# Kernel tuning notes

Measured on AMD Instinct MI355X. Metric: run time of the kernel, lower is better.

The kernel has to match this reference:

```python
import jax, jax.numpy as jnp
import numpy as np

H = 8  # num heads
LORA_SCALE = 1.0


def _lora(x, down, up):
    # down: [rank, in], up: [out, rank]; sigma_mask is None -> ones -> no-op
    return (x @ down.T) @ up.T


def setup_inputs() -> dict:
    key = jax.random.key(0)
    ks = jax.random.split(key, 16)
    B, S, C = 16, 1024, 1280
    Senc, Cenc = 77, 1024
    rank = 4
    s = lambda n: 1.0 / np.sqrt(n)
    inp = {
        "hidden_states": jax.random.normal(ks[0], (B, S, C), jnp.float32),
        "encoder_hidden_states": jax.random.normal(ks[1], (B, Senc, Cenc), jnp.float32),
        "Wq": jax.random.normal(ks[2], (C, C), jnp.float32) * s(C),
        "Wk": jax.random.normal(ks[3], (C, Cenc), jnp.float32) * s(Cenc),
        "Wv": jax.random.normal(ks[4], (C, Cenc), jnp.float32) * s(Cenc),
        "Wo": jax.random.normal(ks[5], (C, C), jnp.float32) * s(C),
        "bo": jnp.zeros((C,), jnp.float32),
        "q_down": jax.random.normal(ks[6], (rank, C), jnp.float32) / rank,
        "q_up": jax.random.normal(ks[7], (C, rank), jnp.float32) * 0.02,
        "k_down": jax.random.normal(ks[8], (rank, Cenc), jnp.float32) / rank,
        "k_up": jax.random.normal(ks[9], (C, rank), jnp.float32) * 0.02,
        "v_down": jax.random.normal(ks[10], (rank, Cenc), jnp.float32) / rank,
        "v_up": jax.random.normal(ks[11], (C, rank), jnp.float32) * 0.02,
        "o_down": jax.random.normal(ks[12], (rank, C), jnp.float32) / rank,
        "o_up": jax.random.normal(ks[13], (C, rank), jnp.float32) * 0.02,
    }
    return inp


def reference(hidden_states, encoder_hidden_states, Wq, Wk, Wv, Wo, bo,
              q_down, q_up, k_down, k_up, v_down, v_up, o_down, o_up):
    B, S, C = hidden_states.shape
    Senc = encoder_hidden_states.shape[1]
    D = C // H
    attn_scale = 1.0 / jnp.sqrt(jnp.asarray(D, hidden_states.dtype))

    q = hidden_states @ Wq.T + LORA_SCALE * _lora(hidden_states, q_down, q_up)
    k = encoder_hidden_states @ Wk.T + LORA_SCALE * _lora(encoder_hidden_states, k_down, k_up)
    v = encoder_hidden_states @ Wv.T + LORA_SCALE * _lora(encoder_hidden_states, v_down, v_up)

    # head_to_batch_dim: [B, S, H*D] -> [B, H, S, D]
    q = q.reshape(B, S, H, D).transpose(0, 2, 1, 3)
    k = k.reshape(B, Senc, H, D).transpose(0, 2, 1, 3)
    v = v.reshape(B, Senc, H, D).transpose(0, 2, 1, 3)

    scores = jnp.einsum("bhqd,bhkd->bhqk", q, k) * attn_scale
    probs = jax.nn.softmax(scores, axis=-1)
    out = jnp.einsum("bhqk,bhkd->bhqd", probs, v)

    # batch_to_head_dim: [B, H, S, D] -> [B, S, H*D]
    out = out.transpose(0, 2, 1, 3).reshape(B, S, C)
    out = out @ Wo.T + bo + LORA_SCALE * _lora(out, o_down, o_up)
    return out
```

## Files before the change

### kernel.cpp

```cpp
#include <hip/hip_runtime.h>

#define NH    8
#define BB    16
#define SQ    1024
#define CC    1280
#define SENC  77
#define CENC  1024
#define DH    160
#define RANK  4

typedef __attribute__((ext_vector_type(8))) short bf16x8;
typedef __attribute__((ext_vector_type(4))) float f32x4;

__device__ inline void split_bf16(float a, unsigned short& hi, unsigned short& lo) {
    unsigned u = __float_as_uint(a);
    hi = (unsigned short)(u >> 16);
    float fhi = __uint_as_float(u & 0xffff0000u);
    float r = a - fhi;
    lo = (unsigned short)(__float_as_uint(r) >> 16);
}

__global__ void fold_kernel(const float* __restrict__ W,
                            const float* __restrict__ up,
                            const float* __restrict__ down,
                            float* __restrict__ out, int N, int K) {
    int idx4 = blockIdx.x * blockDim.x + threadIdx.x;
    int total4 = (N * K) >> 2;
    if (idx4 >= total4) return;
    int i = idx4 << 2;
    int n = i / K;
    int kk = i - n * K;
    float4 acc = *(const float4*)(W + i);
#pragma unroll
    for (int r = 0; r < RANK; ++r) {
        float u = up[n * RANK + r];
        float4 dv = *(const float4*)(down + (size_t)r * K + kk);
        acc.x += u * dv.x; acc.y += u * dv.y;
        acc.z += u * dv.z; acc.w += u * dv.w;
    }
    *(float4*)(out + i) = acc;
}

__global__ void fold_split_kernel(const float* __restrict__ W,
                                  const float* __restrict__ up,
                                  const float* __restrict__ down,
                                  unsigned short* __restrict__ ohi,
                                  unsigned short* __restrict__ olo,
                                  int N, int K) {
    int idx4 = blockIdx.x * blockDim.x + threadIdx.x;
    int total4 = (N * K) >> 2;
    if (idx4 >= total4) return;
    int i = idx4 << 2;
    int n = i / K;
    int kk = i - n * K;
    float4 acc = *(const float4*)(W + i);
#pragma unroll
    for (int r = 0; r < RANK; ++r) {
        float u = up[n * RANK + r];
        float4 dv = *(const float4*)(down + (size_t)r * K + kk);
        acc.x += u * dv.x; acc.y += u * dv.y;
        acc.z += u * dv.z; acc.w += u * dv.w;
    }
    unsigned short h0, h1, h2, h3, l0, l1, l2, l3;
    split_bf16(acc.x, h0, l0); split_bf16(acc.y, h1, l1);
    split_bf16(acc.z, h2, l2); split_bf16(acc.w, h3, l3);
    int2 hv, lv;
    hv.x = (int)((unsigned)h0 | ((unsigned)h1 << 16));
    hv.y = (int)((unsigned)h2 | ((unsigned)h3 << 16));
    lv.x = (int)((unsigned)l0 | ((unsigned)l1 << 16));
    lv.y = (int)((unsigned)l2 | ((unsigned)l3 << 16));
    *(int2*)(ohi + i) = hv;
    *(int2*)(olo + i) = lv;
}

__global__ void split_kernel(const float* __restrict__ x,
                             unsigned short* __restrict__ ohi,
                             unsigned short* __restrict__ olo, int total4) {
    int idx4 = blockIdx.x * blockDim.x + threadIdx.x;
    if (idx4 >= total4) return;
    int i = idx4 << 2;
    float4 a = *(const float4*)(x + i);
    unsigned short h0, h1, h2, h3, l0, l1, l2, l3;
    split_bf16(a.x, h0, l0); split_bf16(a.y, h1, l1);
    split_bf16(a.z, h2, l2); split_bf16(a.w, h3, l3);
    int2 hv, lv;
    hv.x = (int)((unsigned)h0 | ((unsigned)h1 << 16));
    hv.y = (int)((unsigned)h2 | ((unsigned)h3 << 16));
    lv.x = (int)((unsigned)l0 | ((unsigned)l1 << 16));
    lv.y = (int)((unsigned)l2 | ((unsigned)l3 << 16));
    *(int2*)(ohi + i) = hv;
    *(int2*)(olo + i) = lv;
}

__global__ __launch_bounds__(256) void transpose_split_kernel(
    const float* __restrict__ in,
    unsigned short* __restrict__ ohi, unsigned short* __restrict__ olo) {
    __shared__ float t[32][33];
    int tx = threadIdx.x & 31, ty = threadIdx.x >> 5;
    int bx = blockIdx.x, by = blockIdx.y;
#pragma unroll
    for (int r = 0; r < 4; ++r)
        t[ty + 8 * r][tx] = in[(size_t)(by * 32 + ty + 8 * r) * 1280 + bx * 32 + tx];
    __syncthreads();
#pragma unroll
    for (int r = 0; r < 4; ++r) {
        float v = t[tx][ty + 8 * r];
        unsigned short h_, l_;
        split_bf16(v, h_, l_);
        size_t o = (size_t)(bx * 32 + ty + 8 * r) * 1280 + by * 32 + tx;
        ohi[o] = h_; olo[o] = l_;
    }
}

#define GBM 128
#define GBN 128
#define GBK 32

__device__ inline void async_load16(const void* gsrc, void* lds_dst) {
    __builtin_amdgcn_global_load_lds(
        (const __attribute__((address_space(1))) void*)gsrc,
        (__attribute__((address_space(3))) void*)lds_dst, 16, 0, 0);
}

__device__ inline int clampi(int x, int hi) { return x > hi ? hi : x; }

template <int MODE>
__global__ __launch_bounds__(256) void gemm2_kernel(
    const unsigned short* __restrict__ A_hi, const unsigned short* __restrict__ A_lo,
    int lda,
    const unsigned short* __restrict__ W_hi, const unsigned short* __restrict__ W_lo,
    int ldw,
    const float* __restrict__ bias, float* __restrict__ outF,
    unsigned short* __restrict__ oHi, unsigned short* __restrict__ oLo, int ldo,
    int M, int N, int K) {
    __shared__ __align__(16) unsigned short lds[4][GBM][GBK];
    const int tid  = threadIdx.x;
    const int wave = tid >> 6;
    const int lane = tid & 63;

    int m0, n0;
    if constexpr (MODE == 0) {
        n0 = blockIdx.x * GBN; m0 = blockIdx.y * GBM;
    } else if constexpr (MODE == 1) {
        n0 = blockIdx.x * GBN; m0 = 0;
        int z = blockIdx.z, b = z >> 3, hh = z & 7;
        size_t ao = (size_t)(b * SENC) * lda + hh * DH;
        A_hi += ao; A_lo += ao;
        W_hi += hh * DH; W_lo += hh * DH;
        size_t ob = (size_t)(b * 640 + hh * 80) * ldo;
        oHi += ob; oLo += ob;
    } else if constexpr (MODE == 2) {
        n0 = 0; m0 = blockIdx.y * GBM;
        int z = blockIdx.z, b = z >> 3, hh = z & 7;
        A_hi += hh * DH; A_lo += hh * DH;
        size_t wo = (size_t)(b * SENC) * ldw + CC + hh * DH;
        W_hi += wo; W_lo += wo;
        size_t ob = (size_t)b * CC * ldo + hh * 80;
        oHi += ob; oLo += ob;
    } else if constexpr (MODE == 3) {
        int bid = blockIdx.x;
        int w = (bid & 7) * 80 + (bid >> 3);
        int mt = w / 5, nt = w - mt * 5;
        m0 = mt * GBM; n0 = nt * GBN;
        int b = m0 >> 10;
        size_t wo = (size_t)b * 640 * ldw;
        W_hi += wo; W_lo += wo;
    } else {
        int bid = blockIdx.x;
        int w = (bid & 7) * 160 + (bid >> 3);
        int mt = w / 10, nt = w - mt * 10;
        m0 = mt * GBM; n0 = nt * GBN;
        int b = m0 >> 10;
        size_t wo = (size_t)b * CC * ldw;
        W_hi += wo; W_lo += wo;
    }

    const int wr = wave >> 1, wc = wave & 1;
    f32x4 zero = {0.f, 0.f, 0.f, 0.f};
    f32x4 acc[4][4];
#pragma unroll
    for (int i = 0; i < 4; ++i)
#pragma unroll
        for (int j = 0; j < 4; ++j) acc[i][j] = zero;

    const int c0 = wave * 2, c1 = wave * 2 + 1;
    const int rr = lane >> 2;
    const int kc = (lane & 3) * 8;
    const int ra0 = clampi(m0 + c0 * 16 + rr, M - 1);
    const int ra1 = clampi(m0 + c1 * 16 + rr, M - 1);
    const int rw0 = clampi(n0 + c0 * 16 + rr, N - 1);
    const int rw1 = clampi(n0 + c1 * 16 + rr, N - 1);
    const unsigned short* pAh0 = A_hi + (size_t)ra0 * lda + kc;
    const unsigned short* pAh1 = A_hi + (size_t)ra1 * lda + kc;
    const unsigned short* pAl0 = A_lo + (size_t)ra0 * lda + kc;
    const unsigned short* pAl1 = A_lo + (size_t)ra1 * lda + kc;
    const unsigned short* pWh0 = W_hi + (size_t)rw0 * ldw + kc;
    const unsigned short* pWh1 = W_hi + (size_t)rw1 * ldw + kc;
    const unsigned short* pWl0 = W_lo + (size_t)rw0 * ldw + kc;
    const unsigned short* pWl1 = W_lo + (size_t)rw1 * ldw + kc;

    for (int k0 = 0; k0 < K; k0 += GBK) {
        async_load16(pAh0 + k0, &lds[0][c0 * 16][0]);
        async_load16(pAh1 + k0, &lds[0][c1 * 16][0]);
        async_load16(pAl0 + k0, &lds[1][c0 * 16][0]);
        async_load16(pAl1 + k0, &lds[1][c1 * 16][0]);
        async_load16(pWh0 + k0, &lds[2][c0 * 16][0]);
        async_load16(pWh1 + k0, &lds[2][c1 * 16][0]);
        async_load16(pWl0 + k0, &lds[3][c0 * 16][0]);
        async_load16(pWl1 + k0, &lds[3][c1 * 16][0]);
        __syncthreads();

        bf16x8 ah[4], al[4], bh[4], bl[4];
        const int fr = lane & 15;
        const int kb = (lane >> 4) * 8;
#pragma unroll
        for (int i = 0; i < 4; ++i) {
            ah[i] = *(const bf16x8*)&lds[0][wr * 64 + i * 16 + fr][kb];
            al[i] = *(const bf16x8*)&lds[1][wr * 64 + i * 16 + fr][kb];
            bh[i] = *(const bf16x8*)&lds[2][wc * 64 + i * 16 + fr][kb];
            bl[i] = *(const bf16x8*)&lds[3][wc * 64 + i * 16 + fr][kb];
        }
#pragma unroll
        for (int i = 0; i < 4; ++i)
#pragma unroll
            for (int j = 0; j < 4; ++j) {
                acc[i][j] = __builtin_amdgcn_mfma_f32_16x16x32_bf16(ah[i], bh[j], acc[i][j], 0, 0, 0);
                acc[i][j] = __builtin_amdgcn_mfma_f32_16x16x32_bf16(ah[i], bl[j], acc[i][j], 0, 0, 0);
                acc[i][j] = __builtin_amdgcn_mfma_f32_16x16x32_bf16(al[i], bh[j], acc[i][j], 0, 0, 0);
            }
        __syncthreads();
    }

    const int fc = lane & 15;
    const int fr4 = (lane >> 4) * 4;
#pragma unroll
    for (int j = 0; j < 4; ++j) {
        int col = n0 + wc * 64 + j * 16 + fc;
        float bv = 0.f;
        if constexpr (MODE == 4) bv = bias[col];
#pragma unroll
        for (int i = 0; i < 4; ++i) {
            int row = m0 + wr * 64 + i * 16 + fr4;
#pragma unroll
            for (int r = 0; r < 4; ++r) {
                int rowr = row + r;
                float val = acc[i][j][r];
                if constexpr (MODE == 0) {
                    if (rowr < M) {
                        unsigned short vh, vl;
                        split_bf16(val, vh, vl);
                        oHi[(size_t)rowr * ldo + col] = vh;
                        oLo[(size_t)rowr * ldo + col] = vl;
                    }
                } else if constexpr (MODE == 1) {
                    if (rowr < 80) {
                        if (rowr >= SENC) val = 0.f;
                        unsigned short vh, vl;
                        split_bf16(val, vh, vl);
                        oHi[(size_t)rowr * ldo + col] = vh;
                        oLo[(size_t)rowr * ldo + col] = vl;
                    }
                } else if constexpr (MODE == 2) {
                    if (col < 80) {
                        if (col >= SENC) val = 0.f;
                        unsigned short vh, vl;
                        split_bf16(val, vh, vl);
                        oHi[(size_t)rowr * ldo + col] = vh;
                        oLo[(size_t)rowr * ldo + col] = vl;
                    }
                } else if constexpr (MODE == 3) {
                    outF[(size_t)rowr * ldo + col] = val;
                } else {
                    outF[(size_t)rowr * ldo + col] = val + bv;
                }
            }
        }
    }
}

__global__ __launch_bounds__(256) void softmax_kernel(
    const float* __restrict__ S,
    unsigned short* __restrict__ Phi, unsigned short* __restrict__ Plo) {
    const float scale = 0.07905694150420949f;
    int t = blockIdx.x * 256 + threadIdx.x;
    int li = t & 3;
    int g = t >> 2;
    int row = g >> 3, h = g & 7;
    const float* p = S + (size_t)row * 640 + h * 80;

    float v[20];
#pragma unroll
    for (int m = 0; m < 5; ++m) {
        float4 x = *(const float4*)(p + (li + 4 * m) * 4);
        v[m * 4 + 0] = x.x; v[m * 4 + 1] = x.y;
        v[m * 4 + 2] = x.z; v[m * 4 + 3] = x.w;
    }
    float mx = -1e30f;
#pragma unroll
    for (int m = 0; m < 5; ++m)
#pragma unroll
        for (int e = 0; e < 4; ++e) {
            int j = (li + 4 * m) * 4 + e;
            float x = v[m * 4 + e] * scale;
            v[m * 4 + e] = x;
            if (j < SENC) mx = fmaxf(mx, x);
        }
    mx = fmaxf(mx, __shfl_xor(mx, 1));
    mx = fmaxf(mx, __shfl_xor(mx, 2));
    float sum = 0.f;
#pragma unroll
    for (int m = 0; m < 5; ++m)
#pragma unroll
        for (int e = 0; e < 4; ++e) {
            int j = (li + 4 * m) * 4 + e;
            float ex = (j < SENC) ? __expf(v[m * 4 + e] - mx) : 0.f;
            v[m * 4 + e] = ex;
            sum += ex;
        }
    sum += __shfl_xor(sum, 1);
    sum += __shfl_xor(sum, 2);
    float inv = 1.f / sum;

    size_t ob = (size_t)row * 640 + h * 80;
#pragma unroll
    for (int m = 0; m < 5; ++m) {
        unsigned short hh[4], ll[4];
#pragma unroll
        for (int e = 0; e < 4; ++e) split_bf16(v[m * 4 + e] * inv, hh[e], ll[e]);
        ushort4 hv; hv.x = hh[0]; hv.y = hh[1]; hv.z = hh[2]; hv.w = hh[3];
        ushort4 lv; lv.x = ll[0]; lv.y = ll[1]; lv.z = ll[2]; lv.w = ll[3];
        *(ushort4*)(Phi + ob + (li + 4 * m) * 4) = hv;
        *(ushort4*)(Plo + ob + (li + 4 * m) * 4) = lv;
    }
}

extern "C" void kernel_launch(void* const* d_in, const int* in_sizes, int n_in,
                              void* d_out, int out_size, void* d_ws, size_t ws_size,
                              hipStream_t stream) {
    const float* hidden = (const float*)d_in[0];
    const float* enc    = (const float*)d_in[1];
    const float* Wq     = (const float*)d_in[2];
    const float* Wk     = (const float*)d_in[3];
    const float* Wv     = (const float*)d_in[4];
    const float* Wo     = (const float*)d_in[5];
    const float* bo     = (const float*)d_in[6];
    const float* q_down = (const float*)d_in[7];
    const float* q_up   = (const float*)d_in[8];
    const float* k_down = (const float*)d_in[9];
    const float* k_up   = (const float*)d_in[10];
    const float* v_down = (const float*)d_in[11];
    const float* v_up   = (const float*)d_in[12];
    const float* o_down = (const float*)d_in[13];
    const float* o_up   = (const float*)d_in[14];

    char* ws = (char*)d_ws;
    unsigned short* Wo_hi   = (unsigned short*)(ws);
    unsigned short* Wo_lo   = (unsigned short*)(ws + 3276800);
    unsigned short* kv_hi   = (unsigned short*)(ws + 6553600);
    unsigned short* kv_lo   = (unsigned short*)(ws + 12861440);
    unsigned short* Wkv_hi  = (unsigned short*)(ws + 19169280);
    unsigned short* Wkv_lo  = (unsigned short*)(ws + 24412160);
    unsigned short* Nbig_hi = (unsigned short*)(ws + 19169280);
    unsigned short* Nbig_lo = (unsigned short*)(ws + 45383680);
    unsigned short* P_hi    = (unsigned short*)(ws + 19169280);
    unsigned short* P_lo    = (unsigned short*)(ws + 40140800);
    unsigned short* MbT_hi  = (unsigned short*)(ws + 61112320);
    unsigned short* MbT_lo  = (unsigned short*)(ws + 87326720);
    float*          S_f32   = (float*)(ws + 71598080);
    unsigned short* WqT_hi  = (unsigned short*)(ws + 71598080);
    unsigned short* WqT_lo  = (unsigned short*)(ws + 74874880);
    float*          Wq_f32  = (float*)(ws + 78151680);
    unsigned short* enc_hi  = (unsigned short*)(ws + 84705280);
    unsigned short* enc_lo  = (unsigned short*)(ws + 87228416);
    unsigned short* hid_hi  = (unsigned short*)d_out;
    unsigned short* hid_lo  = hid_hi + (size_t)20971520;

    const int M1 = BB * SQ;
    const int M2 = BB * SENC;

    dim3 blk(256);
    fold_split_kernel<<<1600, blk, 0, stream>>>(Wo, o_up, o_down, Wo_hi, Wo_lo, CC, CC);
    fold_kernel<<<1600, blk, 0, stream>>>(Wq, q_up, q_down, Wq_f32, CC, CC);
    transpose_split_kernel<<<dim3(40, 40), blk, 0, stream>>>(Wq_f32, WqT_hi, WqT_lo);
    fold_split_kernel<<<1280, blk, 0, stream>>>(Wk, k_up, k_down, Wkv_hi, Wkv_lo, CC, CENC);
    fold_split_kernel<<<1280, blk, 0, stream>>>(Wv, v_up, v_down,
                                                Wkv_hi + 1310720, Wkv_lo + 1310720, CC, CENC);
    split_kernel<<<1232, blk, 0, stream>>>(enc, enc_hi, enc_lo, (M2 * CENC) / 4);
    split_kernel<<<20480, blk, 0, stream>>>(hidden, hid_hi, hid_lo, (M1 * CC) / 4);

    gemm2_kernel<0><<<dim3(20, 10), blk, 0, stream>>>(
        enc_hi, enc_lo, CENC, Wkv_hi, Wkv_lo, CENC,
        nullptr, nullptr, kv_hi, kv_lo, 2560, M2, 2560, CENC);

    gemm2_kernel<1><<<dim3(10, 1, 128), blk, 0, stream>>>(
        kv_hi, kv_lo, 2560, WqT_hi, WqT_lo, CC,
        nullptr, nullptr, Nbig_hi, Nbig_lo, CC, SENC, CC, DH);

    gemm2_kernel<3><<<640, blk, 0, stream>>>(
        hid_hi, hid_lo, CC, Nbig_hi, Nbig_lo, CC,
        nullptr, S_f32, nullptr, nullptr, 640, M1, 640, CC);

    softmax_kernel<<<2048, blk, 0, stream>>>(S_f32, P_hi, P_lo);

    gemm2_kernel<2><<<dim3(1, 10, 128), blk, 0, stream>>>(
        Wo_hi, Wo_lo, CC, kv_hi, kv_lo, 2560,
        nullptr, nullptr, MbT_hi, MbT_lo, 640, CC, SENC, DH);

    gemm2_kernel<4><<<1280, blk, 0, stream>>>(
        P_hi, P_lo, 640, MbT_hi, MbT_lo, 640,
        bo, (float*)d_out, nullptr, nullptr, CC, M1, CC, 640);
}
```

Baseline: 527.9 us.

## Fuse score GEMM with softmax and merge weight fold/transpose prep kernels

Replaces the separate score GEMM (which wrote fp32 scores) and the softmax kernel with one kernel. It uses 128x160 tiles so each wave owns a full 80-wide head segment and applies softmax in registers, removing the fp32 score round-trip through global memory. It also fuses the Wq LoRA fold into the transpose-split kernel and merges the K/V folds into one launch, saving launches and an intermediate buffer. The trade-off is larger per-thread accumulators (4x5 tiles) and more LDS, which may lower occupancy, plus scattered 2-byte stores for P.

```diff
diff --git a/kernel.cpp b/kernel.cpp
--- a/kernel.cpp
+++ b/kernel.cpp
@@ -18,27 +18,6 @@
     float fhi = __uint_as_float(u & 0xffff0000u);
     float r = a - fhi;
     lo = (unsigned short)(__float_as_uint(r) >> 16);
-}
-
-__global__ void fold_kernel(const float* __restrict__ W,
-                            const float* __restrict__ up,
-                            const float* __restrict__ down,
-                            float* __restrict__ out, int N, int K) {
-    int idx4 = blockIdx.x * blockDim.x + threadIdx.x;
-    int total4 = (N * K) >> 2;
-    if (idx4 >= total4) return;
-    int i = idx4 << 2;
-    int n = i / K;
-    int kk = i - n * K;
-    float4 acc = *(const float4*)(W + i);
-#pragma unroll
-    for (int r = 0; r < RANK; ++r) {
-        float u = up[n * RANK + r];
-        float4 dv = *(const float4*)(down + (size_t)r * K + kk);
-        acc.x += u * dv.x; acc.y += u * dv.y;
-        acc.z += u * dv.z; acc.w += u * dv.w;
-    }
-    *(float4*)(out + i) = acc;
 }
 
 __global__ void fold_split_kernel(const float* __restrict__ W,
@@ -71,6 +50,69 @@
     lv.y = (int)((unsigned)l2 | ((unsigned)l3 << 16));
     *(int2*)(ohi + i) = hv;
     *(int2*)(olo + i) = lv;
+}
+
+__global__ void fold_split_kv_kernel(const float* __restrict__ Wk,
+                                     const float* __restrict__ Wv,
+                                     const float* __restrict__ k_up,
+                                     const float* __restrict__ k_down,
+                                     const float* __restrict__ v_up,
+                                     const float* __restrict__ v_down,
+                                     unsigned short* __restrict__ ohi,
+                                     unsigned short* __restrict__ olo) {
+    int idx4 = blockIdx.x * blockDim.x + threadIdx.x;
+    int i = idx4 << 2;
+    int n = i >> 10;
+    int kk = i & 1023;
+    const float* W; const float* up; const float* down; int nn = n;
+    if (n < CC) { W = Wk; up = k_up; down = k_down; }
+    else        { W = Wv; up = v_up; down = v_down; nn = n - CC; }
+    float4 acc = *(const float4*)(W + (size_t)nn * CENC + kk);
+#pragma unroll
+    for (int r = 0; r < RANK; ++r) {
+        float u = up[nn * RANK + r];
+        float4 dv = *(const float4*)(down + (size_t)r * CENC + kk);
+        acc.x += u * dv.x; acc.y += u * dv.y;
+        acc.z += u * dv.z; acc.w += u * dv.w;
+    }
+    unsigned short h0, h1, h2, h3, l0, l1, l2, l3;
+    split_bf16(acc.x, h0, l0); split_bf16(acc.y, h1, l1);
+    split_bf16(acc.z, h2, l2); split_bf16(acc.w, h3, l3);
+    int2 hv, lv;
+    hv.x = (int)((unsigned)h0 | ((unsigned)h1 << 16));
+    hv.y = (int)((unsigned)h2 | ((unsigned)h3 << 16));
+    lv.x = (int)((unsigned)l0 | ((unsigned)l1 << 16));
+    lv.y = (int)((unsigned)l2 | ((unsigned)l3 << 16));
+    *(int2*)(ohi + i) = hv;
+    *(int2*)(olo + i) = lv;
+}
+
+__global__ __launch_bounds__(256) void foldT_split_kernel(
+    const float* __restrict__ W, const float* __restrict__ up,
+    const float* __restrict__ down,
+    unsigned short* __restrict__ ohi, unsigned short* __restrict__ olo) {
+    __shared__ float t[32][33];
+    int tx = threadIdx.x & 31, ty = threadIdx.x >> 5;
+    int bx = blockIdx.x, by = blockIdx.y;
+    int k = bx * 32 + tx;
+#pragma unroll
+    for (int r4 = 0; r4 < 4; ++r4) {
+        int n = by * 32 + ty + 8 * r4;
+        float v = W[(size_t)n * 1280 + k];
+#pragma unroll
+        for (int r = 0; r < RANK; ++r)
+            v += up[n * RANK + r] * down[r * 1280 + k];
+        t[ty + 8 * r4][tx] = v;
+    }
+    __syncthreads();
+#pragma unroll
+    for (int r4 = 0; r4 < 4; ++r4) {
+        float v = t[tx][ty + 8 * r4];
+        unsigned short h_, l_;
+        split_bf16(v, h_, l_);
+        size_t o = (size_t)(bx * 32 + ty + 8 * r4) * 1280 + by * 32 + tx;
+        ohi[o] = h_; olo[o] = l_;
+    }
 }
 
 __global__ void split_kernel(const float* __restrict__ x,
@@ -90,26 +132,6 @@
     lv.y = (int)((unsigned)l2 | ((unsigned)l3 << 16));
     *(int2*)(ohi + i) = hv;
     *(int2*)(olo + i) = lv;
-}
-
-__global__ __launch_bounds__(256) void transpose_split_kernel(
-    const float* __restrict__ in,
-    unsigned short* __restrict__ ohi, unsigned short* __restrict__ olo) {
-    __shared__ float t[32][33];
-    int tx = threadIdx.x & 31, ty = threadIdx.x >> 5;
-    int bx = blockIdx.x, by = blockIdx.y;
-#pragma unroll
-    for (int r = 0; r < 4; ++r)
-        t[ty + 8 * r][tx] = in[(size_t)(by * 32 + ty + 8 * r) * 1280 + bx * 32 + tx];
-    __syncthreads();
-#pragma unroll
-    for (int r = 0; r < 4; ++r) {
-        float v = t[tx][ty + 8 * r];
-        unsigned short h_, l_;
-        split_bf16(v, h_, l_);
-        size_t o = (size_t)(bx * 32 + ty + 8 * r) * 1280 + by * 32 + tx;
-        ohi[o] = h_; olo[o] = l_;
-    }
 }
 
 #define GBM 128
@@ -157,14 +179,6 @@
         W_hi += wo; W_lo += wo;
         size_t ob = (size_t)b * CC * ldo + hh * 80;
         oHi += ob; oLo += ob;
-    } else if constexpr (MODE == 3) {
-        int bid = blockIdx.x;
-        int w = (bid & 7) * 80 + (bid >> 3);
-        int mt = w / 5, nt = w - mt * 5;
-        m0 = mt * GBM; n0 = nt * GBN;
-        int b = m0 >> 10;
-        size_t wo = (size_t)b * 640 * ldw;
-        W_hi += wo; W_lo += wo;
     } else {
         int bid = blockIdx.x;
         int w = (bid & 7) * 160 + (bid >> 3);
@@ -268,8 +282,6 @@
                         oHi[(size_t)rowr * ldo + col] = vh;
                         oLo[(size_t)rowr * ldo + col] = vl;
                     }
-                } else if constexpr (MODE == 3) {
-                    outF[(size_t)rowr * ldo + col] = val;
                 } else {
                     outF[(size_t)rowr * ldo + col] = val + bv;
                 }
@@ -278,59 +290,118 @@
     }
 }
 
-__global__ __launch_bounds__(256) void softmax_kernel(
-    const float* __restrict__ S,
-    unsigned short* __restrict__ Phi, unsigned short* __restrict__ Plo) {
+__global__ __launch_bounds__(256) void sgemm_softmax_kernel(
+    const unsigned short* __restrict__ A_hi, const unsigned short* __restrict__ A_lo,
+    const unsigned short* __restrict__ Nbig_hi, const unsigned short* __restrict__ Nbig_lo,
+    unsigned short* __restrict__ P_hi, unsigned short* __restrict__ P_lo) {
+    __shared__ __align__(16) unsigned short sLDS[18432];
+    const int tid = threadIdx.x;
+    const int wave = tid >> 6;
+    const int lane = tid & 63;
+    const int fr = lane & 15;
+    const int g = lane >> 4;
     const float scale = 0.07905694150420949f;
-    int t = blockIdx.x * 256 + threadIdx.x;
-    int li = t & 3;
-    int g = t >> 2;
-    int row = g >> 3, h = g & 7;
-    const float* p = S + (size_t)row * 640 + h * 80;
-
-    float v[20];
-#pragma unroll
-    for (int m = 0; m < 5; ++m) {
-        float4 x = *(const float4*)(p + (li + 4 * m) * 4);
-        v[m * 4 + 0] = x.x; v[m * 4 + 1] = x.y;
-        v[m * 4 + 2] = x.z; v[m * 4 + 3] = x.w;
-    }
-    float mx = -1e30f;
-#pragma unroll
-    for (int m = 0; m < 5; ++m)
-#pragma unroll
-        for (int e = 0; e < 4; ++e) {
-            int j = (li + 4 * m) * 4 + e;
-            float x = v[m * 4 + e] * scale;
-            v[m * 4 + e] = x;
-            if (j < SENC) mx = fmaxf(mx, x);
+
+    int bid = blockIdx.x;
+    int w = (bid & 7) * 64 + (bid >> 3);
+    int mt = w >> 2, nt = w & 3;
+    const int m0 = mt * 128;
+    const int n0 = nt * 160;
+    const int b = mt >> 3;
+    const unsigned short* W_hi = Nbig_hi + (size_t)b * 640 * CC;
+    const unsigned short* W_lo = Nbig_lo + (size_t)b * 640 * CC;
+
+    const int wr = wave >> 1, wc = wave & 1;
+
+    const int rr = lane >> 2;
+    const int kcs = ((lane & 3) ^ ((lane >> 3) & 3)) * 8;
+    const unsigned short* gsrc[9];
+    int ldst[9];
+#pragma unroll
+    for (int q = 0; q < 9; ++q) {
+        int c = wave * 9 + q;
+        const unsigned short* base; int ld, row0, toff, lc;
+        if (c < 8)       { base = A_hi; ld = CC; row0 = m0; toff = 0;     lc = c; }
+        else if (c < 16) { base = A_lo; ld = CC; row0 = m0; toff = 4096;  lc = c - 8; }
+        else if (c < 26) { base = W_hi; ld = CC; row0 = n0; toff = 8192;  lc = c - 16; }
+        else             { base = W_lo; ld = CC; row0 = n0; toff = 13312; lc = c - 26; }
+        gsrc[q] = base + (size_t)(row0 + lc * 16 + rr) * ld + kcs;
+        ldst[q] = toff + lc * 512;
+    }
+
+    f32x4 zero = {0.f, 0.f, 0.f, 0.f};
+    f32x4 acc[4][5];
+#pragma unroll
+    for (int i = 0; i < 4; ++i)
+#pragma unroll
+        for (int j = 0; j < 5; ++j) acc[i][j] = zero;
+
+    const int kbsw = (g ^ ((fr >> 1) & 3)) * 8;
+
+    for (int k0 = 0; k0 < CC; k0 += 32) {
+#pragma unroll
+        for (int q = 0; q < 9; ++q)
+            async_load16(gsrc[q] + k0, &sLDS[ldst[q]]);
+        __syncthreads();
+
+        bf16x8 ah[4], al[4];
+#pragma unroll
+        for (int i = 0; i < 4; ++i) {
+            int r = wr * 64 + i * 16 + fr;
+            ah[i] = *(const bf16x8*)&sLDS[r * 32 + kbsw];
+            al[i] = *(const bf16x8*)&sLDS[4096 + r * 32 + kbsw];
         }
-    mx = fmaxf(mx, __shfl_xor(mx, 1));
-    mx = fmaxf(mx, __shfl_xor(mx, 2));
-    float sum = 0.f;
-#pragma unroll
-    for (int m = 0; m < 5; ++m)
-#pragma unroll
-        for (int e = 0; e < 4; ++e) {
-            int j = (li + 4 * m) * 4 + e;
-            float ex = (j < SENC) ? __expf(v[m * 4 + e] - mx) : 0.f;
-            v[m * 4 + e] = ex;
-            sum += ex;
+#pragma unroll
+        for (int j = 0; j < 5; ++j) {
+            int rb = wc * 80 + j * 16 + fr;
+            bf16x8 bh = *(const bf16x8*)&sLDS[8192 + rb * 32 + kbsw];
+            bf16x8 bl = *(const bf16x8*)&sLDS[13312 + rb * 32 + kbsw];
+#pragma unroll
+            for (int i = 0; i < 4; ++i) {
+                acc[i][j] = __builtin_amdgcn_mfma_f32_16x16x32_bf16(ah[i], bh, acc[i][j], 0, 0, 0);
+                acc[i][j] = __builtin_amdgcn_mfma_f32_16x16x32_bf16(ah[i], bl, acc[i][j], 0, 0, 0);
+                acc[i][j] = __builtin_amdgcn_mfma_f32_16x16x32_bf16(al[i], bh, acc[i][j], 0, 0, 0);
+            }
         }
-    sum += __shfl_xor(sum, 1);
-    sum += __shfl_xor(sum, 2);
-    float inv = 1.f / sum;
-
-    size_t ob = (size_t)row * 640 + h * 80;
-#pragma unroll
-    for (int m = 0; m < 5; ++m) {
-        unsigned short hh[4], ll[4];
-#pragma unroll
-        for (int e = 0; e < 4; ++e) split_bf16(v[m * 4 + e] * inv, hh[e], ll[e]);
-        ushort4 hv; hv.x = hh[0]; hv.y = hh[1]; hv.z = hh[2]; hv.w = hh[3];
-        ushort4 lv; lv.x = ll[0]; lv.y = ll[1]; lv.z = ll[2]; lv.w = ll[3];
-        *(ushort4*)(Phi + ob + (li + 4 * m) * 4) = hv;
-        *(ushort4*)(Plo + ob + (li + 4 * m) * 4) = lv;
+        __syncthreads();
+    }
+
+    const int fc = fr;
+    const bool maskme = (fc >= 13);
+#pragma unroll
+    for (int i = 0; i < 4; ++i) {
+#pragma unroll
+        for (int r = 0; r < 4; ++r) {
+            float m = -1e30f;
+#pragma unroll
+            for (int j = 0; j < 5; ++j) {
+                float v = acc[i][j][r] * scale;
+                if (j == 4 && maskme) v = -1e30f;
+                acc[i][j][r] = v;
+                m = fmaxf(m, v);
+            }
+#pragma unroll
+            for (int msk = 1; msk < 16; msk <<= 1) m = fmaxf(m, __shfl_xor(m, msk));
+            float sum = 0.f;
+#pragma unroll
+            for (int j = 0; j < 5; ++j) {
+                float e = (j == 4 && maskme) ? 0.f : __expf(acc[i][j][r] - m);
+                acc[i][j][r] = e;
+                sum += e;
+            }
+#pragma unroll
+            for (int msk = 1; msk < 16; msk <<= 1) sum += __shfl_xor(sum, msk);
+            float inv = 1.f / sum;
+            int row = m0 + wr * 64 + i * 16 + g * 4 + r;
+            size_t ob = (size_t)row * 640 + n0 + wc * 80 + fc;
+#pragma unroll
+            for (int j = 0; j < 5; ++j) {
+                unsigned short ph, pl;
+                split_bf16(acc[i][j][r] * inv, ph, pl);
+                P_hi[ob + j * 16] = ph;
+                P_lo[ob + j * 16] = pl;
+            }
+        }
     }
 }
 
@@ -362,16 +433,14 @@
     unsigned short* Wkv_lo  = (unsigned short*)(ws + 24412160);
     unsigned short* Nbig_hi = (unsigned short*)(ws + 19169280);
     unsigned short* Nbig_lo = (unsigned short*)(ws + 45383680);
-    unsigned short* P_hi    = (unsigned short*)(ws + 19169280);
-    unsigned short* P_lo    = (unsigned short*)(ws + 40140800);
-    unsigned short* MbT_hi  = (unsigned short*)(ws + 61112320);
-    unsigned short* MbT_lo  = (unsigned short*)(ws + 87326720);
-    float*          S_f32   = (float*)(ws + 71598080);
+    unsigned short* MbT_hi  = (unsigned short*)(ws + 19169280);
+    unsigned short* MbT_lo  = (unsigned short*)(ws + 45383680);
     unsigned short* WqT_hi  = (unsigned short*)(ws + 71598080);
     unsigned short* WqT_lo  = (unsigned short*)(ws + 74874880);
-    float*          Wq_f32  = (float*)(ws + 78151680);
-    unsigned short* enc_hi  = (unsigned short*)(ws + 84705280);
-    unsigned short* enc_lo  = (unsigned short*)(ws + 87228416);
+    unsigned short* enc_hi  = (unsigned short*)(ws + 78151680);
+    unsigned short* enc_lo  = (unsigned short*)(ws + 80674816);
+    unsigned short* P_hi    = (unsigned short*)(ws + 78151680);
+    unsigned short* P_lo    = (unsigned short*)(ws + 99123200);
     unsigned short* hid_hi  = (unsigned short*)d_out;
     unsigned short* hid_lo  = hid_hi + (size_t)20971520;
 
@@ -380,11 +449,9 @@
 
     dim3 blk(256);
     fold_split_kernel<<<1600, blk, 0, stream>>>(Wo, o_up, o_down, Wo_hi, Wo_lo, CC, CC);
-    fold_kernel<<<1600, blk, 0, stream>>>(Wq, q_up, q_down, Wq_f32, CC, CC);
-    transpose_split_kernel<<<dim3(40, 40), blk, 0, stream>>>(Wq_f32, WqT_hi, WqT_lo);
-    fold_split_kernel<<<1280, blk, 0, stream>>>(Wk, k_up, k_down, Wkv_hi, Wkv_lo, CC, CENC);
-    fold_split_kernel<<<1280, blk, 0, stream>>>(Wv, v_up, v_down,
-                                                Wkv_hi + 1310720, Wkv_lo + 1310720, CC, CENC);
+    foldT_split_kernel<<<dim3(40, 40), blk, 0, stream>>>(Wq, q_up, q_down, WqT_hi, WqT_lo);
+    fold_split_kv_kernel<<<2560, blk, 0, stream>>>(Wk, Wv, k_up, k_down, v_up, v_down,
+                                                   Wkv_hi, Wkv_lo);
     split_kernel<<<1232, blk, 0, stream>>>(enc, enc_hi, enc_lo, (M2 * CENC) / 4);
     split_kernel<<<20480, blk, 0, stream>>>(hidden, hid_hi, hid_lo, (M1 * CC) / 4);
 
@@ -396,11 +463,8 @@
         kv_hi, kv_lo, 2560, WqT_hi, WqT_lo, CC,
         nullptr, nullptr, Nbig_hi, Nbig_lo, CC, SENC, CC, DH);
 
-    gemm2_kernel<3><<<640, blk, 0, stream>>>(
-        hid_hi, hid_lo, CC, Nbig_hi, Nbig_lo, CC,
-        nullptr, S_f32, nullptr, nullptr, 640, M1, 640, CC);
-
-    softmax_kernel<<<2048, blk, 0, stream>>>(S_f32, P_hi, P_lo);
+    sgemm_softmax_kernel<<<512, blk, 0, stream>>>(
+        hid_hi, hid_lo, Nbig_hi, Nbig_lo, P_hi, P_lo);
 
     gemm2_kernel<2><<<dim3(1, 10, 128), blk, 0, stream>>>(
         Wo_hi, Wo_lo, CC, kv_hi, kv_lo, 2560,
```

Measured after the change: 484.7 us. 8.2% less time.
